# Kernel tuning notes

Hardware: AMD Instinct MI355X
Metric: run time of the kernel (lower is better)

## Reference

```python
import jax, jax.numpy as jnp
import numpy as np

ALPHA = 0.2  # LeakyReLU negative slope
NEG = -9e15


def setup_inputs() -> dict:
    key = jax.random.key(0)
    k1, k2, k3, k4 = jax.random.split(key, 4)
    N, F_in, F_out = 8192, 512, 64
    h = jax.random.normal(k1, (N, F_in), dtype=jnp.float32)
    adj = jax.random.randint(k2, (N, N), 0, 2, dtype=jnp.int32)
    # xavier_uniform with gain=1.414
    def xavier(k, shape, gain=1.414):
        fan_in, fan_out = shape[0], shape[1]
        bound = gain * np.sqrt(6.0 / (fan_in + fan_out))
        return jax.random.uniform(k, shape, jnp.float32, -bound, bound)
    W = xavier(k3, (F_in, F_out))
    a = xavier(k4, (2 * F_out, 1))
    return {"h": h, "adj": adj, "W": W, "a": a}


def reference(h, adj, W, a):
    F_out = W.shape[1]
    Wh = h @ W                                   # [N, F_out]
    # e_ij = LeakyReLU([Wh_i || Wh_j] . a) = LeakyReLU(Wh.a1 + (Wh.a2)^T)
    e1 = Wh @ a[:F_out, 0]                       # [N]
    e2 = Wh @ a[F_out:, 0]                       # [N]
    e = jax.nn.leaky_relu(e1[:, None] + e2[None, :], ALPHA)  # [N, N]
    e = jnp.where(adj > 0, e, NEG)
    attention = jax.nn.softmax(e, axis=1)        # dropout p=0.0 -> identity
    h_prime = attention @ Wh                     # [N, F_out]
    return jax.nn.elu(h_prime)                   # concat=True
```

## Files before the change

### kernel.cpp

```cpp
#include <hip/hip_runtime.h>
#include <hip/hip_bf16.h>
#include <stdint.h>

typedef __attribute__((ext_vector_type(8))) short short8;
typedef __attribute__((ext_vector_type(4))) float f32x4;

#define NSLICE 8
#define SLICE_J 1024
#define CHUNKS 16
#define L2E 1.44269504f

static __device__ __forceinline__ short f2bf(float f) {
    unsigned int u = __float_as_uint(f);
    u += 0x7fffu + ((u >> 16) & 1u);
    return (short)(u >> 16);
}

static __device__ __forceinline__ short welem(int a, float e2s, float e1s, float& lsum) {
    float x = e1s + e2s;
    x = fmaxf(x, 0.f) + 0.2f * fminf(x, 0.f);
    float w = __builtin_amdgcn_exp2f(x);
    w = (a > 0) ? w : 0.f;
    lsum += w;
    return f2bf(w);
}

__global__ __launch_bounds__(256)
void gat_wh(const float* __restrict__ h, const float* __restrict__ W,
            const float* __restrict__ a, short* __restrict__ whT,
            float* __restrict__ e1, float* __restrict__ e2)
{
    __shared__ float sW[128][64];
    const int tid  = threadIdx.x;
    const int lane = tid & 63;
    const int wave = tid >> 6;
    const int row0 = blockIdx.x * 16 + wave * 4;

    float acc[4] = {0.f, 0.f, 0.f, 0.f};
#pragma unroll
    for (int t = 0; t < 4; ++t) {
        const int c0 = t * 128;
        {
            const float4* src = reinterpret_cast<const float4*>(W + c0 * 64);
            float4* dst = reinterpret_cast<float4*>(&sW[0][0]);
#pragma unroll
            for (int k = 0; k < 8; ++k) dst[tid + k * 256] = src[tid + k * 256];
        }
        __syncthreads();
#pragma unroll 4
        for (int ci = 0; ci < 128; ++ci) {
            const float wv = sW[ci][lane];
#pragma unroll
            for (int r = 0; r < 4; ++r)
                acc[r] += h[(size_t)(row0 + r) * 512 + c0 + ci] * wv;
        }
        __syncthreads();
    }

    const float a1v = a[lane];
    const float a2v = a[64 + lane];
    const int f    = lane >> 4;
    const int r16n = lane & 15;
#pragma unroll
    for (int r = 0; r < 4; ++r) {
        float p1 = acc[r] * a1v;
        float p2 = acc[r] * a2v;
#pragma unroll
        for (int off = 32; off; off >>= 1) {
            p1 += __shfl_xor(p1, off);
            p2 += __shfl_xor(p2, off);
        }
        if (lane == 0) { e1[row0 + r] = p1; e2[row0 + r] = p2; }
        const int j = row0 + r;
        const int kin = j & 63;
        const int frag = (kin >> 5) & 1, qk = (kin >> 3) & 3, t = kin & 7;
        whT[(size_t)(j >> 6) * 4096 + (f * 2 + frag) * 512 + qk * 128 + r16n * 8 + t]
            = f2bf(acc[r]);
    }
}

__global__ __launch_bounds__(256)
void gat_attn(const int* __restrict__ adj, const short* __restrict__ whT,
              const float* __restrict__ e1, const float* __restrict__ e2,
              float* __restrict__ lpart, float* __restrict__ opart)
{
    __shared__ float se2[SLICE_J];
    const int bid = blockIdx.x;
    const int s   = bid & (NSLICE - 1);
    const int rb  = bid >> 3;
    const int tid = threadIdx.x;

    {
        float4 v = *reinterpret_cast<const float4*>(e2 + s * SLICE_J + tid * 4);
        v.x *= L2E; v.y *= L2E; v.z *= L2E; v.w *= L2E;
        *reinterpret_cast<float4*>(se2 + tid * 4) = v;
    }
    __syncthreads();

    const int lane = tid & 63;
    const int wave = tid >> 6;
    const int quad = lane >> 4;
    const int r16  = lane & 15;
    const int rowBase = rb * 64 + wave * 16;
    const int row  = rowBase + r16;
    const float e1s = e1[row] * L2E;
    const size_t adjRow = (size_t)row * 8192 + (size_t)s * SLICE_J;

    float lsum = 0.f;
    f32x4 acc[4];
#pragma unroll
    for (int ff = 0; ff < 4; ++ff) acc[ff] = (f32x4){0.f, 0.f, 0.f, 0.f};

    for (int ch = 0; ch < CHUNKS; ++ch) {
        const int j0 = ch * 64 + quad * 8;
        const int4 A0 = *reinterpret_cast<const int4*>(adj + adjRow + j0);
        const int4 A1 = *reinterpret_cast<const int4*>(adj + adjRow + j0 + 4);
        const int4 A2 = *reinterpret_cast<const int4*>(adj + adjRow + j0 + 32);
        const int4 A3 = *reinterpret_cast<const int4*>(adj + adjRow + j0 + 36);
        const float4 E0 = *reinterpret_cast<const float4*>(se2 + j0);
        const float4 E1 = *reinterpret_cast<const float4*>(se2 + j0 + 4);
        const float4 E2 = *reinterpret_cast<const float4*>(se2 + j0 + 32);
        const float4 E3 = *reinterpret_cast<const float4*>(se2 + j0 + 36);

        short8 af0, af1;
        af0[0] = welem(A0.x, E0.x, e1s, lsum);
        af0[1] = welem(A0.y, E0.y, e1s, lsum);
        af0[2] = welem(A0.z, E0.z, e1s, lsum);
        af0[3] = welem(A0.w, E0.w, e1s, lsum);
        af0[4] = welem(A1.x, E1.x, e1s, lsum);
        af0[5] = welem(A1.y, E1.y, e1s, lsum);
        af0[6] = welem(A1.z, E1.z, e1s, lsum);
        af0[7] = welem(A1.w, E1.w, e1s, lsum);
        af1[0] = welem(A2.x, E2.x, e1s, lsum);
        af1[1] = welem(A2.y, E2.y, e1s, lsum);
        af1[2] = welem(A2.z, E2.z, e1s, lsum);
        af1[3] = welem(A2.w, E2.w, e1s, lsum);
        af1[4] = welem(A3.x, E3.x, e1s, lsum);
        af1[5] = welem(A3.y, E3.y, e1s, lsum);
        af1[6] = welem(A3.z, E3.z, e1s, lsum);
        af1[7] = welem(A3.w, E3.w, e1s, lsum);

        const short* wtile = whT + (size_t)(s * 16 + ch) * 4096 + lane * 8;
#pragma unroll
        for (int ff = 0; ff < 4; ++ff) {
            const short8 b0 = *reinterpret_cast<const short8*>(wtile + (ff * 2 + 0) * 512);
            const short8 b1 = *reinterpret_cast<const short8*>(wtile + (ff * 2 + 1) * 512);
            acc[ff] = __builtin_amdgcn_mfma_f32_16x16x32_bf16(af0, b0, acc[ff], 0, 0, 0);
            acc[ff] = __builtin_amdgcn_mfma_f32_16x16x32_bf16(af1, b1, acc[ff], 0, 0, 0);
        }
    }

    lsum += __shfl_xor(lsum, 16);
    lsum += __shfl_xor(lsum, 32);
    if (lane < 16) lpart[s * 8192 + rowBase + lane] = lsum;

#pragma unroll
    for (int ff = 0; ff < 4; ++ff) {
#pragma unroll
        for (int rg = 0; rg < 4; ++rg) {
            const int orow = rowBase + quad * 4 + rg;
            const int ocol = ff * 16 + r16;
            opart[((size_t)s * 8192 + orow) * 64 + ocol] = acc[ff][rg];
        }
    }
}

__global__ __launch_bounds__(256)
void gat_combine(const float* __restrict__ lpart, const float* __restrict__ opart,
                 float* __restrict__ out)
{
    const int gid = blockIdx.x * 256 + threadIdx.x;
    const int row = gid >> 6;
    const int f   = gid & 63;

    float lsum = 0.f, osum = 0.f;
#pragma unroll
    for (int s = 0; s < NSLICE; ++s) {
        lsum += lpart[s * 8192 + row];
        osum += opart[((size_t)s * 8192 + row) * 64 + f];
    }
    const float v = osum / lsum;
    out[gid] = (v > 0.f) ? v : (__expf(v) - 1.f);
}

extern "C" void kernel_launch(void* const* d_in, const int* in_sizes, int n_in,
                              void* d_out, int out_size, void* d_ws, size_t ws_size,
                              hipStream_t stream) {
    const float* h   = (const float*)d_in[0];
    const int*   adj = (const int*)d_in[1];
    const float* W   = (const float*)d_in[2];
    const float* a   = (const float*)d_in[3];
    float* out = (float*)d_out;

    char* ws = (char*)d_ws;
    short* whT   = (short*)ws;
    float* e1    = (float*)(ws + (1u << 20));
    float* e2    = (float*)(ws + (1u << 20) + (32u << 10));
    float* lpart = (float*)(ws + (1u << 20) + (64u << 10));
    float* opart = (float*)(ws + (2u << 20));

    gat_wh<<<512, 256, 0, stream>>>(h, W, a, whT, e1, e2);
    gat_attn<<<128 * NSLICE, 256, 0, stream>>>(adj, whT, e1, e2, lpart, opart);
    gat_combine<<<out_size / 256, 256, 0, stream>>>(lpart, opart, out);
}
```

Baseline: 434.9 us.

## Double-buffer adjacency loads into LDS via async global_load_lds prefetch

The per-chunk adjacency int4 loads in the attention kernel now go through direct global-to-LDS async loads into a per-wave double buffer. The next chunk is prefetched while the current one is computed. This is meant to hide the latency of streaming the 256 MB adjacency matrix behind the exp and MFMA work. The cost is extra LDS (32 KB per block), which may lower occupancy. The vmcnt(0) wait also stalls on the whT global loads, and there is no barrier between waves, which is fine only because each wave uses its own buffers.

Result: no change. 438.1 us (+0.7%).

```diff
diff --git a/kernel.cpp b/kernel.cpp
--- a/kernel.cpp
+++ b/kernel.cpp
@@ -23,6 +23,12 @@
     w = (a > 0) ? w : 0.f;
     lsum += w;
     return f2bf(w);
+}
+
+typedef __attribute__((address_space(3))) int lds_int;
+typedef __attribute__((address_space(1))) const int glb_int;
+static __device__ __forceinline__ void gload_lds16(const int* g, int* l) {
+    __builtin_amdgcn_global_load_lds((glb_int*)g, (lds_int*)l, 16, 0, 0);
 }
 
 __global__ __launch_bounds__(256)
@@ -85,6 +91,7 @@
               float* __restrict__ lpart, float* __restrict__ opart)
 {
     __shared__ float se2[SLICE_J];
+    __shared__ int sadj[2][4][4][256];
     const int bid = blockIdx.x;
     const int s   = bid & (NSLICE - 1);
     const int rb  = bid >> 3;
@@ -104,23 +111,39 @@
     const int rowBase = rb * 64 + wave * 16;
     const int row  = rowBase + r16;
     const float e1s = e1[row] * L2E;
-    const size_t adjRow = (size_t)row * 8192 + (size_t)s * SLICE_J;
+    const int* arow = adj + (size_t)row * 8192 + (size_t)s * SLICE_J + quad * 8;
 
     float lsum = 0.f;
     f32x4 acc[4];
 #pragma unroll
     for (int ff = 0; ff < 4; ++ff) acc[ff] = (f32x4){0.f, 0.f, 0.f, 0.f};
 
+    gload_lds16(arow + 0,  &sadj[0][wave][0][0]);
+    gload_lds16(arow + 4,  &sadj[0][wave][1][0]);
+    gload_lds16(arow + 32, &sadj[0][wave][2][0]);
+    gload_lds16(arow + 36, &sadj[0][wave][3][0]);
+
     for (int ch = 0; ch < CHUNKS; ++ch) {
+        const int b = ch & 1;
+        asm volatile("s_waitcnt vmcnt(0)" ::: "memory");
+        const int4 A0 = *reinterpret_cast<const int4*>(&sadj[b][wave][0][lane * 4]);
+        const int4 A1 = *reinterpret_cast<const int4*>(&sadj[b][wave][1][lane * 4]);
+        const int4 A2 = *reinterpret_cast<const int4*>(&sadj[b][wave][2][lane * 4]);
+        const int4 A3 = *reinterpret_cast<const int4*>(&sadj[b][wave][3][lane * 4]);
         const int j0 = ch * 64 + quad * 8;
-        const int4 A0 = *reinterpret_cast<const int4*>(adj + adjRow + j0);
-        const int4 A1 = *reinterpret_cast<const int4*>(adj + adjRow + j0 + 4);
-        const int4 A2 = *reinterpret_cast<const int4*>(adj + adjRow + j0 + 32);
-        const int4 A3 = *reinterpret_cast<const int4*>(adj + adjRow + j0 + 36);
         const float4 E0 = *reinterpret_cast<const float4*>(se2 + j0);
         const float4 E1 = *reinterpret_cast<const float4*>(se2 + j0 + 4);
         const float4 E2 = *reinterpret_cast<const float4*>(se2 + j0 + 32);
         const float4 E3 = *reinterpret_cast<const float4*>(se2 + j0 + 36);
+        __builtin_amdgcn_sched_barrier(0);
+
+        if (ch + 1 < CHUNKS) {
+            const int* an = arow + (ch + 1) * 64;
+            gload_lds16(an + 0,  &sadj[b ^ 1][wave][0][0]);
+            gload_lds16(an + 4,  &sadj[b ^ 1][wave][1][0]);
+            gload_lds16(an + 32, &sadj[b ^ 1][wave][2][0]);
+            gload_lds16(an + 36, &sadj[b ^ 1][wave][3][0]);
+        }
 
         short8 af0, af1;
         af0[0] = welem(A0.x, E0.x, e1s, lsum);
```

## Fuse split-K combine into attention kernel via in-block LDS reduction

Applied to the files above, without the earlier changes.

Restructures gat_attn so each 512-thread block owns 16 rows and its 8 waves each handle one 1024-column slice. The partial sums are reduced through shared memory and the ELU output is written directly. This removes the separate combine kernel and the global round trip of partial outputs (about 16 MB of opart). In exchange each block loads all of e2 into LDS and uses much more shared memory per block. The grid also shrinks to 512 blocks, which may lower occupancy.

Result: slower. 448.3 us (+3.1%).

```diff
diff --git a/kernel.cpp b/kernel.cpp
--- a/kernel.cpp
+++ b/kernel.cpp
@@ -5,9 +5,6 @@
 typedef __attribute__((ext_vector_type(8))) short short8;
 typedef __attribute__((ext_vector_type(4))) float f32x4;
 
-#define NSLICE 8
-#define SLICE_J 1024
-#define CHUNKS 16
 #define L2E 1.44269504f
 
 static __device__ __forceinline__ short f2bf(float f) {
@@ -79,21 +76,22 @@
     }
 }
 
-__global__ __launch_bounds__(256)
+__global__ __launch_bounds__(512)
 void gat_attn(const int* __restrict__ adj, const short* __restrict__ whT,
               const float* __restrict__ e1, const float* __restrict__ e2,
-              float* __restrict__ lpart, float* __restrict__ opart)
+              float* __restrict__ out)
 {
-    __shared__ float se2[SLICE_J];
+    __shared__ float se2[8192];
+    __shared__ float red[8][16][64];
+    __shared__ float redl[8][16];
     const int bid = blockIdx.x;
-    const int s   = bid & (NSLICE - 1);
-    const int rb  = bid >> 3;
     const int tid = threadIdx.x;
 
-    {
-        float4 v = *reinterpret_cast<const float4*>(e2 + s * SLICE_J + tid * 4);
+#pragma unroll
+    for (int k = 0; k < 4; ++k) {
+        float4 v = *reinterpret_cast<const float4*>(e2 + k * 2048 + tid * 4);
         v.x *= L2E; v.y *= L2E; v.z *= L2E; v.w *= L2E;
-        *reinterpret_cast<float4*>(se2 + tid * 4) = v;
+        *reinterpret_cast<float4*>(se2 + k * 2048 + tid * 4) = v;
     }
     __syncthreads();
 
@@ -101,26 +99,27 @@
     const int wave = tid >> 6;
     const int quad = lane >> 4;
     const int r16  = lane & 15;
-    const int rowBase = rb * 64 + wave * 16;
+    const int rowBase = bid * 16;
     const int row  = rowBase + r16;
     const float e1s = e1[row] * L2E;
-    const size_t adjRow = (size_t)row * 8192 + (size_t)s * SLICE_J;
+    const size_t adjRow = (size_t)row * 8192 + (size_t)wave * 1024;
+    const float* se2w = se2 + wave * 1024;
 
     float lsum = 0.f;
     f32x4 acc[4];
 #pragma unroll
     for (int ff = 0; ff < 4; ++ff) acc[ff] = (f32x4){0.f, 0.f, 0.f, 0.f};
 
-    for (int ch = 0; ch < CHUNKS; ++ch) {
+    for (int ch = 0; ch < 16; ++ch) {
         const int j0 = ch * 64 + quad * 8;
         const int4 A0 = *reinterpret_cast<const int4*>(adj + adjRow + j0);
         const int4 A1 = *reinterpret_cast<const int4*>(adj + adjRow + j0 + 4);
         const int4 A2 = *reinterpret_cast<const int4*>(adj + adjRow + j0 + 32);
         const int4 A3 = *reinterpret_cast<const int4*>(adj + adjRow + j0 + 36);
-        const float4 E0 = *reinterpret_cast<const float4*>(se2 + j0);
-        const float4 E1 = *reinterpret_cast<const float4*>(se2 + j0 + 4);
-        const float4 E2 = *reinterpret_cast<const float4*>(se2 + j0 + 32);
-        const float4 E3 = *reinterpret_cast<const float4*>(se2 + j0 + 36);
+        const float4 E0 = *reinterpret_cast<const float4*>(se2w + j0);
+        const float4 E1 = *reinterpret_cast<const float4*>(se2w + j0 + 4);
+        const float4 E2 = *reinterpret_cast<const float4*>(se2w + j0 + 32);
+        const float4 E3 = *reinterpret_cast<const float4*>(se2w + j0 + 36);
 
         short8 af0, af1;
         af0[0] = welem(A0.x, E0.x, e1s, lsum);
@@ -140,7 +139,7 @@
         af1[6] = welem(A3.z, E3.z, e1s, lsum);
         af1[7] = welem(A3.w, E3.w, e1s, lsum);
 
-        const short* wtile = whT + (size_t)(s * 16 + ch) * 4096 + lane * 8;
+        const short* wtile = whT + (size_t)(wave * 16 + ch) * 4096 + lane * 8;
 #pragma unroll
         for (int ff = 0; ff < 4; ++ff) {
             const short8 b0 = *reinterpret_cast<const short8*>(wtile + (ff * 2 + 0) * 512);
@@ -152,35 +151,25 @@
 
     lsum += __shfl_xor(lsum, 16);
     lsum += __shfl_xor(lsum, 32);
-    if (lane < 16) lpart[s * 8192 + rowBase + lane] = lsum;
+    if (lane < 16) redl[wave][lane] = lsum;
 
 #pragma unroll
-    for (int ff = 0; ff < 4; ++ff) {
+    for (int ff = 0; ff < 4; ++ff)
 #pragma unroll
-        for (int rg = 0; rg < 4; ++rg) {
-            const int orow = rowBase + quad * 4 + rg;
-            const int ocol = ff * 16 + r16;
-            opart[((size_t)s * 8192 + orow) * 64 + ocol] = acc[ff][rg];
-        }
+        for (int rg = 0; rg < 4; ++rg)
+            red[wave][quad * 4 + rg][ff * 16 + r16] = acc[ff][rg];
+    __syncthreads();
+
+#pragma unroll
+    for (int e = 0; e < 2; ++e) {
+        const int idx = tid + e * 512;
+        const int r = idx >> 6, f = idx & 63;
+        float ls = 0.f, os = 0.f;
+#pragma unroll
+        for (int w = 0; w < 8; ++w) { ls += redl[w][r]; os += red[w][r][f]; }
+        const float v = os / ls;
+        out[(size_t)(rowBase + r) * 64 + f] = (v > 0.f) ? v : (__expf(v) - 1.f);
     }
-}
-
-__global__ __launch_bounds__(256)
-void gat_combine(const float* __restrict__ lpart, const float* __restrict__ opart,
-                 float* __restrict__ out)
-{
-    const int gid = blockIdx.x * 256 + threadIdx.x;
-    const int row = gid >> 6;
-    const int f   = gid & 63;
-
-    float lsum = 0.f, osum = 0.f;
-#pragma unroll
-    for (int s = 0; s < NSLICE; ++s) {
-        lsum += lpart[s * 8192 + row];
-        osum += opart[((size_t)s * 8192 + row) * 64 + f];
-    }
-    const float v = osum / lsum;
-    out[gid] = (v > 0.f) ? v : (__expf(v) - 1.f);
 }
 
 extern "C" void kernel_launch(void* const* d_in, const int* in_sizes, int n_in,
@@ -193,13 +182,10 @@
     float* out = (float*)d_out;
 
     char* ws = (char*)d_ws;
-    short* whT   = (short*)ws;
-    float* e1    = (float*)(ws + (1u << 20));
-    float* e2    = (float*)(ws + (1u << 20) + (32u << 10));
-    float* lpart = (float*)(ws + (1u << 20) + (64u << 10));
-    float* opart = (float*)(ws + (2u << 20));
+    short* whT = (short*)ws;
+    float* e1  = (float*)(ws + (1u << 20));
+    float* e2  = (float*)(ws + (1u << 20) + (32u << 10));
 
     gat_wh<<<512, 256, 0, stream>>>(h, W, a, whT, e1, e2);
-    gat_attn<<<128 * NSLICE, 256, 0, stream>>>(adj, whT, e1, e2, lpart, opart);
-    gat_combine<<<out_size / 256, 256, 0, stream>>>(lpart, opart, out);
+    gat_attn<<<512, 512, 0, stream>>>(adj, whT, e1, e2, out);
 }
```
